# Kernel tuning notes

Hardware: AMD Instinct MI355X
Metric: run time of the kernel (lower is better)

The kernel has to match this reference:

```python
import jax, jax.numpy as jnp
import numpy as np

BN_EPS = 1e-5


def setup_inputs() -> dict:
    key = jax.random.key(0)
    k1, k2, k3 = jax.random.split(key, 3)
    B, IN, H, C = 65536, 784, 1024, 10
    x = jax.random.normal(k1, (B, IN), dtype=jnp.float32)
    # Kaiming-ish real-valued latent weights
    w1 = jax.random.normal(k2, (H, IN), dtype=jnp.float32) * 0.03
    w2 = jax.random.normal(k3, (C, H), dtype=jnp.float32) * 0.03
    gamma = jnp.ones((H,), dtype=jnp.float32)
    beta = jnp.zeros((H,), dtype=jnp.float32)
    return {"x": x, "w1": w1, "w2": w2, "gamma": gamma, "beta": beta}


def _bin_weight(w):
    # XNOR-Net weight binarization: per-output-row alpha * sign(w)
    alpha = jnp.mean(jnp.abs(w), axis=1, keepdims=True)  # [out, 1]
    return alpha * jnp.sign(w)


def reference(x, w1, w2, gamma, beta):
    x = x.reshape(x.shape[0], -1)                      # [B, 784]
    h = x @ _bin_weight(w1).T                          # [B, 1024]
    # BatchNorm1d, training mode: batch mean / biased variance
    mu = jnp.mean(h, axis=0)
    var = jnp.mean(jnp.square(h - mu), axis=0)
    h = gamma * (h - mu) * jax.lax.rsqrt(var + BN_EPS) + beta
    a = jnp.sign(h)                                    # binarized activation
    out = a @ _bin_weight(w2).T                        # [B, 10]
    return out
```

## Files before the change

### kernel.cpp

```cpp
#include <hip/hip_runtime.h>
#include <hip/hip_fp16.h>

#define BATCH   65536
#define IN_DIM  784
#define KPAD    800
#define K2      1600
#define H_DIM   1024
#define C_DIM   10
#define BN_EPS  1e-5f
#define NT      (K2 / 32)

typedef _Float16 half8 __attribute__((ext_vector_type(8)));
typedef _Float16 half4 __attribute__((ext_vector_type(4)));
typedef float    f32x4 __attribute__((ext_vector_type(4)));

#if defined(__has_builtin)
#if __has_builtin(__builtin_amdgcn_global_load_lds)
#define HAVE_ASYNC 1
#endif
#endif
#ifndef HAVE_ASYNC
#define HAVE_ASYNC 0
#endif

__device__ __forceinline__ void stage16(const _Float16* g, _Float16* ldsBase, int lane) {
#if HAVE_ASYNC
  __builtin_amdgcn_global_load_lds((const __attribute__((address_space(1))) void*)g,
                                   (__attribute__((address_space(3))) void*)ldsBase,
                                   16, 0, 0);
#else
  *(half8*)(ldsBase + lane * 8) = *(const half8*)g;
#endif
}

__global__ __launch_bounds__(256) void split_x(const float* __restrict__ x,
                                               _Float16* __restrict__ X2) {
  const long tid = (long)blockIdx.x * 256 + threadIdx.x;
  const long row = tid / 200;
  const int  q   = (int)(tid - row * 200);
  const int  k   = q * 4;
  half4 hi = {}, lo = {};
  if (k < IN_DIM) {
    const f32x4 v = *(const f32x4*)&x[row * IN_DIM + k];
#pragma unroll
    for (int i = 0; i < 4; ++i) {
      const _Float16 h = (_Float16)v[i];
      hi[i] = h;
      lo[i] = (_Float16)(v[i] - (float)h);
    }
  }
  _Float16* dst = X2 + row * K2 + k;
  *(half4*)dst = hi;
  *(half4*)(dst + KPAD) = lo;
}

__global__ __launch_bounds__(256) void prep_w(const float* __restrict__ w1,
                                              const float* __restrict__ w2,
                                              float* __restrict__ alpha1,
                                              _Float16* __restrict__ S2,
                                              float* __restrict__ bw2) {
  __shared__ float red[4];
  const int tid = threadIdx.x, lane = tid & 63, wave = tid >> 6;
  const int j = blockIdx.x;
  if (j < H_DIM) {
    const float* wr = w1 + (long)j * IN_DIM;
    float s = 0.f;
    for (int k = tid; k < IN_DIM; k += 256) s += fabsf(wr[k]);
#pragma unroll
    for (int off = 32; off > 0; off >>= 1) s += __shfl_xor(s, off, 64);
    if (lane == 0) red[wave] = s;
    __syncthreads();
    if (tid == 0) alpha1[j] = (red[0] + red[1] + red[2] + red[3]) * (1.f / IN_DIM);
    _Float16* dr = S2 + (long)j * K2;
    for (int k = tid; k < KPAD; k += 256) {
      const float v = (k < IN_DIM) ? wr[k] : 0.f;
      const _Float16 sg = (_Float16)((v > 0.f) ? 1.f : ((v < 0.f) ? -1.f : 0.f));
      dr[k] = sg;
      dr[KPAD + k] = sg;
    }
  } else {
    const int c = j - H_DIM;
    const float* wr = w2 + (long)c * H_DIM;
    float s = 0.f;
    for (int k = tid; k < H_DIM; k += 256) s += fabsf(wr[k]);
#pragma unroll
    for (int off = 32; off > 0; off >>= 1) s += __shfl_xor(s, off, 64);
    if (lane == 0) red[wave] = s;
    __syncthreads();
    const float alpha = (red[0] + red[1] + red[2] + red[3]) * (1.f / H_DIM);
    for (int k = tid; k < H_DIM; k += 256) {
      const float v = wr[k];
      const float sg = (v > 0.f) ? 1.f : ((v < 0.f) ? -1.f : 0.f);
      bw2[(long)c * H_DIM + k] = alpha * sg;
    }
  }
}

__global__ __launch_bounds__(512, 2) void gemm1(const _Float16* __restrict__ X2,
                                                const _Float16* __restrict__ S2,
                                                const float* __restrict__ alpha1,
                                                float* __restrict__ H,
                                                float* __restrict__ colsum,
                                                float* __restrict__ colsumsq) {
  __shared__ _Float16 lds[4 * 16384];
  const int tid  = threadIdx.x;
  const int lane = tid & 63;
  const int w    = tid >> 6;
  const int wr   = w >> 2;
  const int wc   = w & 3;

  const int b     = blockIdx.x;
  const int xcd   = b & 7;
  const int local = b >> 3;
  const long m0   = (long)(xcd * 32 + (local >> 2)) * 256;
  const int  n0   = (local & 3) * 256;

  const int c8 = ((lane & 3) ^ ((lane >> 3) & 3)) * 8;
  const _Float16* aG = X2 + (m0 + w * 32 + (lane >> 2)) * K2 + c8;
  const _Float16* bG = S2 + (long)(n0 + w * 32 + (lane >> 2)) * K2 + c8;
  const int ldsW0 = (w * 32) * 32;
  const int ldsW1 = (w * 32 + 16) * 32;

  const int fr = lane & 15;
  const int kc = lane >> 4;
  const int cp = (kc ^ ((fr >> 1) & 3)) * 8;
  const int aoff = (wr * 128 + fr) * 32 + cp;
  const int boff = (wc * 64 + fr) * 32 + cp;

  f32x4 acc[8][4] = {};

#pragma unroll
  for (int kt = 0; kt < 3; ++kt) {
    _Float16* Ap = &lds[kt * 16384];
    _Float16* Bp = Ap + 8192;
    stage16(aG + kt * 32, Ap + ldsW0, lane);
    stage16(aG + 16 * K2 + kt * 32, Ap + ldsW1, lane);
    stage16(bG + kt * 32, Bp + ldsW0, lane);
    stage16(bG + 16 * K2 + kt * 32, Bp + ldsW1, lane);
  }

  for (int t = 0; t < NT; ++t) {
    _Float16* Asl = &lds[(t & 3) * 16384];
    _Float16* Bsl = Asl + 8192;
    const int ks = (t + 3 < NT) ? (t + 3) * 32 : (NT - 1) * 32;
    _Float16* Ap = &lds[((t + 3) & 3) * 16384];
    _Float16* Bp = Ap + 8192;

    asm volatile("s_waitcnt vmcnt(8)" ::: "memory");
    __builtin_amdgcn_s_barrier();
    asm volatile("" ::: "memory");

    half8 af[4], bf[4];
#pragma unroll
    for (int ni = 0; ni < 4; ++ni) bf[ni] = *(const half8*)&Bsl[boff + ni * 512];
#pragma unroll
    for (int mi = 0; mi < 4; ++mi) af[mi] = *(const half8*)&Asl[aoff + mi * 512];
    stage16(aG + ks, Ap + ldsW0, lane);
    stage16(aG + 16 * K2 + ks, Ap + ldsW1, lane);
    __builtin_amdgcn_s_setprio(1);
#pragma unroll
    for (int mi = 0; mi < 4; ++mi)
#pragma unroll
      for (int ni = 0; ni < 4; ++ni)
        acc[mi][ni] = __builtin_amdgcn_mfma_f32_16x16x32_f16(af[mi], bf[ni], acc[mi][ni], 0, 0, 0);
    __builtin_amdgcn_s_setprio(0);
    __builtin_amdgcn_s_barrier();

#pragma unroll
    for (int mi = 0; mi < 4; ++mi) af[mi] = *(const half8*)&Asl[aoff + (mi + 4) * 512];
    stage16(bG + ks, Bp + ldsW0, lane);
    stage16(bG + 16 * K2 + ks, Bp + ldsW1, lane);
    __builtin_amdgcn_s_setprio(1);
#pragma unroll
    for (int mi = 0; mi < 4; ++mi)
#pragma unroll
      for (int ni = 0; ni < 4; ++ni)
        acc[mi + 4][ni] = __builtin_amdgcn_mfma_f32_16x16x32_f16(af[mi], bf[ni], acc[mi + 4][ni], 0, 0, 0);
    __builtin_amdgcn_s_setprio(0);
  }

  asm volatile("s_waitcnt vmcnt(0)" ::: "memory");

  const int rq = (lane >> 4) * 4;
#pragma unroll
  for (int ni = 0; ni < 4; ++ni) {
    const int col = n0 + wc * 64 + ni * 16 + fr;
    const float a1 = alpha1[col];
    float s = 0.f, q = 0.f;
#pragma unroll
    for (int mi = 0; mi < 8; ++mi) {
#pragma unroll
      for (int r = 0; r < 4; ++r) {
        const long row = m0 + wr * 128 + mi * 16 + rq + r;
        const float v = acc[mi][ni][r] * a1;
        H[row * H_DIM + col] = v;
        s += v;
        q += v * v;
      }
    }
    s += __shfl_xor(s, 16, 64);
    s += __shfl_xor(s, 32, 64);
    q += __shfl_xor(q, 16, 64);
    q += __shfl_xor(q, 32, 64);
    if ((lane >> 4) == 0) {
      atomicAdd(&colsum[col], s);
      atomicAdd(&colsumsq[col], q);
    }
  }
}

__global__ __launch_bounds__(256) void final_k(const float* __restrict__ H,
                                               const float* __restrict__ colsum,
                                               const float* __restrict__ colsumsq,
                                               const float* __restrict__ gamma,
                                               const float* __restrict__ beta,
                                               const float* __restrict__ bw2,
                                               float* __restrict__ out) {
  __shared__ float cs[H_DIM], ts[H_DIM];
  __shared__ float w2s[C_DIM * H_DIM];
  const int tid = threadIdx.x, lane = tid & 63, wave = tid >> 6;
  for (int j = tid; j < H_DIM; j += 256) {
    const float mu  = colsum[j] * (1.f / BATCH);
    const float var = colsumsq[j] * (1.f / BATCH) - mu * mu;
    const float c   = gamma[j] * rsqrtf(var + BN_EPS);
    cs[j] = c;
    ts[j] = beta[j] - c * mu;
  }
  for (int i = tid; i < C_DIM * H_DIM; i += 256) w2s[i] = bw2[i];
  __syncthreads();

  const long row = (long)blockIdx.x * 256 + wave * 64 + lane;
  const float* hr = H + row * H_DIM;
  float p[C_DIM] = {};
#pragma unroll 8
  for (int j4 = 0; j4 < H_DIM / 4; ++j4) {
    const f32x4 v  = *(const f32x4*)&hr[j4 * 4];
    const f32x4 cv = *(const f32x4*)&cs[j4 * 4];
    const f32x4 tv = *(const f32x4*)&ts[j4 * 4];
    f32x4 a;
#pragma unroll
    for (int i = 0; i < 4; ++i) {
      const float hv = v[i] * cv[i] + tv[i];
      a[i] = (hv > 0.f) ? 1.f : ((hv < 0.f) ? -1.f : 0.f);
    }
#pragma unroll
    for (int oc = 0; oc < C_DIM; ++oc) {
      const f32x4 wv = *(const f32x4*)&w2s[oc * H_DIM + j4 * 4];
      p[oc] += a[0] * wv[0] + a[1] * wv[1] + a[2] * wv[2] + a[3] * wv[3];
    }
  }
  float* orow = out + row * C_DIM;
#pragma unroll
  for (int oc = 0; oc < C_DIM; ++oc) orow[oc] = p[oc];
}

extern "C" void kernel_launch(void* const* d_in, const int* in_sizes, int n_in,
                              void* d_out, int out_size, void* d_ws, size_t ws_size,
                              hipStream_t stream) {
  const float* x     = (const float*)d_in[0];
  const float* w1    = (const float*)d_in[1];
  const float* w2    = (const float*)d_in[2];
  const float* gamma = (const float*)d_in[3];
  const float* beta  = (const float*)d_in[4];
  float* out = (float*)d_out;

  char* ws = (char*)d_ws;
  _Float16* X2     = (_Float16*)(ws + 0);
  float*    H      = (float*)  (ws + 209715200LL);
  _Float16* S2     = (_Float16*)(ws + 478150656LL);
  float*    BW2    = (float*)  (ws + 481427456LL);
  float*    ALPHA1 = (float*)  (ws + 481468416LL);
  float*    COLS   = (float*)  (ws + 481472512LL);
  float*    COLQ   = (float*)  (ws + 481476608LL);

  hipMemsetAsync(COLS, 0, 2 * H_DIM * sizeof(float), stream);
  split_x<<<(BATCH * 200) / 256, 256, 0, stream>>>(x, X2);
  prep_w<<<H_DIM + C_DIM, 256, 0, stream>>>(w1, w2, ALPHA1, S2, BW2);
  gemm1<<<1024, 512, 0, stream>>>(X2, S2, ALPHA1, H, COLS, COLQ);
  final_k<<<BATCH / 256, 256, 0, stream>>>(H, COLS, COLQ, gamma, beta, BW2, out);
}
```

Baseline: 665.2 us.

## Coalesce H reads in final kernel and deepen GEMM LDS pipeline to five stages

```diff
diff --git a/kernel.cpp b/kernel.cpp
--- a/kernel.cpp
+++ b/kernel.cpp
@@ -102,7 +102,7 @@
                                                 float* __restrict__ H,
                                                 float* __restrict__ colsum,
                                                 float* __restrict__ colsumsq) {
-  __shared__ _Float16 lds[4 * 16384];
+  __shared__ _Float16 lds[5 * 16384];
   const int tid  = threadIdx.x;
   const int lane = tid & 63;
   const int w    = tid >> 6;
@@ -130,7 +130,7 @@
   f32x4 acc[8][4] = {};
 
 #pragma unroll
-  for (int kt = 0; kt < 3; ++kt) {
+  for (int kt = 0; kt < 4; ++kt) {
     _Float16* Ap = &lds[kt * 16384];
     _Float16* Bp = Ap + 8192;
     stage16(aG + kt * 32, Ap + ldsW0, lane);
@@ -139,24 +139,26 @@
     stage16(bG + 16 * K2 + kt * 32, Bp + ldsW1, lane);
   }
 
+  int scur = 0;
+  int spre = 4;
   for (int t = 0; t < NT; ++t) {
-    _Float16* Asl = &lds[(t & 3) * 16384];
+    _Float16* Asl = &lds[scur * 16384];
     _Float16* Bsl = Asl + 8192;
-    const int ks = (t + 3 < NT) ? (t + 3) * 32 : (NT - 1) * 32;
-    _Float16* Ap = &lds[((t + 3) & 3) * 16384];
+    const int ks = (t + 4 < NT) ? (t + 4) * 32 : (NT - 1) * 32;
+    _Float16* Ap = &lds[spre * 16384];
     _Float16* Bp = Ap + 8192;
 
-    asm volatile("s_waitcnt vmcnt(8)" ::: "memory");
+    asm volatile("s_waitcnt vmcnt(12)" ::: "memory");
     __builtin_amdgcn_s_barrier();
     asm volatile("" ::: "memory");
 
-    half8 af[4], bf[4];
-#pragma unroll
-    for (int ni = 0; ni < 4; ++ni) bf[ni] = *(const half8*)&Bsl[boff + ni * 512];
-#pragma unroll
-    for (int mi = 0; mi < 4; ++mi) af[mi] = *(const half8*)&Asl[aoff + mi * 512];
     stage16(aG + ks, Ap + ldsW0, lane);
     stage16(aG + 16 * K2 + ks, Ap + ldsW1, lane);
+    half8 af[4], bf[4];
+#pragma unroll
+    for (int ni = 0; ni < 4; ++ni) bf[ni] = *(const half8*)&Bsl[boff + ni * 512];
+#pragma unroll
+    for (int mi = 0; mi < 4; ++mi) af[mi] = *(const half8*)&Asl[aoff + mi * 512];
     __builtin_amdgcn_s_setprio(1);
 #pragma unroll
     for (int mi = 0; mi < 4; ++mi)
@@ -166,10 +168,10 @@
     __builtin_amdgcn_s_setprio(0);
     __builtin_amdgcn_s_barrier();
 
-#pragma unroll
-    for (int mi = 0; mi < 4; ++mi) af[mi] = *(const half8*)&Asl[aoff + (mi + 4) * 512];
     stage16(bG + ks, Bp + ldsW0, lane);
     stage16(bG + 16 * K2 + ks, Bp + ldsW1, lane);
+#pragma unroll
+    for (int mi = 0; mi < 4; ++mi) af[mi] = *(const half8*)&Asl[aoff + (mi + 4) * 512];
     __builtin_amdgcn_s_setprio(1);
 #pragma unroll
     for (int mi = 0; mi < 4; ++mi)
@@ -177,6 +179,9 @@
       for (int ni = 0; ni < 4; ++ni)
         acc[mi + 4][ni] = __builtin_amdgcn_mfma_f32_16x16x32_f16(af[mi], bf[ni], acc[mi + 4][ni], 0, 0, 0);
     __builtin_amdgcn_s_setprio(0);
+
+    scur = (scur == 4) ? 0 : scur + 1;
+    spre = (spre == 4) ? 0 : spre + 1;
   }
 
   asm volatile("s_waitcnt vmcnt(0)" ::: "memory");
@@ -209,49 +214,71 @@
   }
 }
 
-__global__ __launch_bounds__(256) void final_k(const float* __restrict__ H,
-                                               const float* __restrict__ colsum,
-                                               const float* __restrict__ colsumsq,
-                                               const float* __restrict__ gamma,
-                                               const float* __restrict__ beta,
-                                               const float* __restrict__ bw2,
-                                               float* __restrict__ out) {
-  __shared__ float cs[H_DIM], ts[H_DIM];
-  __shared__ float w2s[C_DIM * H_DIM];
+__global__ __launch_bounds__(256, 2) void final_k(const float* __restrict__ H,
+                                                  const float* __restrict__ colsum,
+                                                  const float* __restrict__ colsumsq,
+                                                  const float* __restrict__ gamma,
+                                                  const float* __restrict__ beta,
+                                                  const float* __restrict__ bw2,
+                                                  float* __restrict__ out) {
   const int tid = threadIdx.x, lane = tid & 63, wave = tid >> 6;
-  for (int j = tid; j < H_DIM; j += 256) {
-    const float mu  = colsum[j] * (1.f / BATCH);
-    const float var = colsumsq[j] * (1.f / BATCH) - mu * mu;
-    const float c   = gamma[j] * rsqrtf(var + BN_EPS);
-    cs[j] = c;
-    ts[j] = beta[j] - c * mu;
-  }
-  for (int i = tid; i < C_DIM * H_DIM; i += 256) w2s[i] = bw2[i];
-  __syncthreads();
-
-  const long row = (long)blockIdx.x * 256 + wave * 64 + lane;
-  const float* hr = H + row * H_DIM;
-  float p[C_DIM] = {};
-#pragma unroll 8
-  for (int j4 = 0; j4 < H_DIM / 4; ++j4) {
-    const f32x4 v  = *(const f32x4*)&hr[j4 * 4];
-    const f32x4 cv = *(const f32x4*)&cs[j4 * 4];
-    const f32x4 tv = *(const f32x4*)&ts[j4 * 4];
-    f32x4 a;
+  f32x4 w2r[4][C_DIM];
+  f32x4 csr[4], tsr[4];
+#pragma unroll
+  for (int c4 = 0; c4 < 4; ++c4) {
+    const int col = c4 * 256 + lane * 4;
+    const f32x4 s  = *(const f32x4*)&colsum[col];
+    const f32x4 q  = *(const f32x4*)&colsumsq[col];
+    const f32x4 g  = *(const f32x4*)&gamma[col];
+    const f32x4 bt = *(const f32x4*)&beta[col];
+    f32x4 c, t;
 #pragma unroll
     for (int i = 0; i < 4; ++i) {
-      const float hv = v[i] * cv[i] + tv[i];
-      a[i] = (hv > 0.f) ? 1.f : ((hv < 0.f) ? -1.f : 0.f);
+      const float mu  = s[i] * (1.f / BATCH);
+      const float var = q[i] * (1.f / BATCH) - mu * mu;
+      c[i] = g[i] * rsqrtf(var + BN_EPS);
+      t[i] = bt[i] - c[i] * mu;
+    }
+    csr[c4] = c;
+    tsr[c4] = t;
+#pragma unroll
+    for (int oc = 0; oc < C_DIM; ++oc)
+      w2r[c4][oc] = *(const f32x4*)&bw2[oc * H_DIM + col];
+  }
+
+  const long wrow0 = ((long)blockIdx.x * 4 + wave) * 8;
+#pragma unroll 1
+  for (int r = 0; r < 8; ++r) {
+    const long row = wrow0 + r;
+    const float* hr = H + row * H_DIM;
+    f32x4 h[4];
+#pragma unroll
+    for (int c4 = 0; c4 < 4; ++c4) h[c4] = *(const f32x4*)&hr[c4 * 256 + lane * 4];
+    float p[C_DIM] = {};
+#pragma unroll
+    for (int c4 = 0; c4 < 4; ++c4) {
+      f32x4 a;
+#pragma unroll
+      for (int i = 0; i < 4; ++i) {
+        const float hv = h[c4][i] * csr[c4][i] + tsr[c4][i];
+        a[i] = (hv > 0.f) ? 1.f : ((hv < 0.f) ? -1.f : 0.f);
+      }
+#pragma unroll
+      for (int oc = 0; oc < C_DIM; ++oc) {
+        const f32x4 wv = w2r[c4][oc];
+        p[oc] += a[0] * wv[0] + a[1] * wv[1] + a[2] * wv[2] + a[3] * wv[3];
+      }
     }
 #pragma unroll
     for (int oc = 0; oc < C_DIM; ++oc) {
-      const f32x4 wv = *(const f32x4*)&w2s[oc * H_DIM + j4 * 4];
-      p[oc] += a[0] * wv[0] + a[1] * wv[1] + a[2] * wv[2] + a[3] * wv[3];
-    }
-  }
-  float* orow = out + row * C_DIM;
-#pragma unroll
-  for (int oc = 0; oc < C_DIM; ++oc) orow[oc] = p[oc];
+#pragma unroll
+      for (int off = 32; off > 0; off >>= 1) p[oc] += __shfl_xor(p[oc], off, 64);
+    }
+    if (lane == 0) {
+#pragma unroll
+      for (int oc = 0; oc < C_DIM; ++oc) out[row * C_DIM + oc] = p[oc];
+    }
+  }
 }
 
 extern "C" void kernel_launch(void* const* d_in, const int* in_sizes, int n_in,
@@ -277,5 +304,5 @@
   split_x<<<(BATCH * 200) / 256, 256, 0, stream>>>(x, X2);
   prep_w<<<H_DIM + C_DIM, 256, 0, stream>>>(w1, w2, ALPHA1, S2, BW2);
   gemm1<<<1024, 512, 0, stream>>>(X2, S2, ALPHA1, H, COLS, COLQ);
-  final_k<<<BATCH / 256, 256, 0, stream>>>(H, COLS, COLQ, gamma, beta, BW2, out);
-}
+  final_k<<<BATCH / 32, 256, 0, stream>>>(H, COLS, COLQ, gamma, beta, BW2, out);
+}
```

Result: faster. 615.0 us (-7.5%).
